# Optimization experiments

Hardware: AMD Instinct MI355X
Metric: run time of the kernel (lower is better)

## Reference

```python
import jax, jax.numpy as jnp
import numpy as np
from functools import partial

VOCAB, EMB, HID, B, T, K = 30000, 256, 512, 128, 256, 12
START, STOP = 10, 11


def lstm_scan(xs, mask, W_ih, W_hh, b_ih, b_hh, h0, c0):
    """xs: [T,B,E], mask: [T,B] bool. PyTorch gate order i,f,g,o. Masked steps carry state (packed-seq semantics)."""
    def step(carry, inp):
        h, c = carry
        x_t, m_t = inp
        gates = x_t @ W_ih.T + h @ W_hh.T + (b_ih + b_hh)  # [B,4H]
        i, f, g, o = jnp.split(gates, 4, axis=-1)
        c_new = jax.nn.sigmoid(f) * c + jax.nn.sigmoid(i) * jnp.tanh(g)
        h_new = jax.nn.sigmoid(o) * jnp.tanh(c_new)
        m = m_t[:, None]
        h = jnp.where(m, h_new, h)
        c = jnp.where(m, c_new, c)
        return (h, c), h
    _, hs = jax.lax.scan(step, (h0, c0), (xs, mask))
    return hs  # [T,B,H]


def crf_log_partition(emissions, mask, trans):
    """emissions: [T,B,K], mask: [T,B]. Vectorized log-sum-exp forward algorithm."""
    b, k = emissions.shape[1], emissions.shape[2]
    alpha0 = jnp.full((b, k), -10000.0, emissions.dtype).at[:, START].set(0.0)
    def step(alpha, inp):
        emit_t, m_t = inp
        # alpha_new[b,j] = logsumexp_i(alpha[b,i] + trans[j,i]) + emit[b,j]
        scores = alpha[:, None, :] + trans[None, :, :]  # [B,Knext,Kprev]
        alpha_new = jax.nn.logsumexp(scores, axis=-1) + emit_t
        return jnp.where(m_t[:, None], alpha_new, alpha), None
    alpha, _ = jax.lax.scan(step, alpha0, (emissions, mask))
    return jax.nn.logsumexp(alpha + trans[STOP][None, :], axis=-1)  # [B]


def crf_gold_score(emissions_bt, tags, lengths, trans):
    """emissions_bt: [B,T,K]. Gold path score with <start> prepended and <stop> transition."""
    b, t = tags.shape
    tags_ext = jnp.concatenate([jnp.full((b, 1), START, tags.dtype), tags], axis=1)  # [B,T+1]
    prev, nxt = tags_ext[:, :-1], tags_ext[:, 1:]  # [B,T]
    trans_s = trans[nxt, prev]  # [B,T]
    emit_s = jnp.take_along_axis(emissions_bt, nxt[:, :, None], axis=2)[:, :, 0]  # [B,T]
    valid = jnp.arange(t)[None, :] < lengths[:, None]  # [B,T]
    score = jnp.sum(jnp.where(valid, trans_s + emit_s, 0.0), axis=1)
    last_tag = jnp.take_along_axis(tags, (lengths - 1)[:, None], axis=1)[:, 0]
    return score + trans[STOP, last_tag]


def setup_inputs() -> dict:
    key = jax.random.key(0)
    ks = jax.random.split(key, 16)
    s = 0.1
    x = jax.random.randint(ks[0], (B, T), 0, VOCAB)
    lengths = jax.random.randint(ks[1], (B,), 1, T + 1)
    tags = jax.random.randint(ks[2], (B, T), 0, K - 2)  # real labels only
    embedding = jax.random.normal(ks[3], (VOCAB, EMB), jnp.float32) * s
    W_ih_f = jax.random.normal(ks[4], (4 * HID, EMB), jnp.float32) * s
    W_hh_f = jax.random.normal(ks[5], (4 * HID, HID), jnp.float32) * s
    b_ih_f = jax.random.normal(ks[6], (4 * HID,), jnp.float32) * s
    b_hh_f = jax.random.normal(ks[7], (4 * HID,), jnp.float32) * s
    W_ih_b = jax.random.normal(ks[8], (4 * HID, EMB), jnp.float32) * s
    W_hh_b = jax.random.normal(ks[9], (4 * HID, HID), jnp.float32) * s
    b_ih_b = jax.random.normal(ks[10], (4 * HID,), jnp.float32) * s
    b_hh_b = jax.random.normal(ks[11], (4 * HID,), jnp.float32) * s
    fc_W = jax.random.normal(ks[12], (K, 2 * HID), jnp.float32) * s
    fc_b = jnp.zeros((K,), jnp.float32)
    trans = jax.random.normal(ks[13], (K, K), jnp.float32) * s
    trans = trans.at[START, :].set(-10000.0).at[:, STOP].set(-10000.0)
    h0 = jax.random.normal(ks[14], (2, B, HID), jnp.float32) * s
    c0 = jax.random.normal(ks[15], (2, B, HID), jnp.float32) * s
    return dict(x=x, lengths=lengths, tags=tags, embedding=embedding,
                W_ih_f=W_ih_f, W_hh_f=W_hh_f, b_ih_f=b_ih_f, b_hh_f=b_hh_f,
                W_ih_b=W_ih_b, W_hh_b=W_hh_b, b_ih_b=b_ih_b, b_hh_b=b_hh_b,
                fc_W=fc_W, fc_b=fc_b, trans=trans, h0=h0, c0=c0)


def reference(x, lengths, tags, embedding, W_ih_f, W_hh_f, b_ih_f, b_hh_f,
              W_ih_b, W_hh_b, b_ih_b, b_hh_b, fc_W, fc_b, trans, h0, c0):
    # neg_log_likelihood: BiLSTM emission feats -> CRF logZ - gold score. Dropout = eval (identity).
    emb = embedding[x]                 # [B,T,E]
    xs = emb.transpose(1, 0, 2)        # [T,B,E] time-major
    t = xs.shape[0]
    mask = jnp.arange(t)[:, None] < lengths[None, :]  # [T,B]
    hs_f = lstm_scan(xs, mask, W_ih_f, W_hh_f, b_ih_f, b_hh_f, h0[0], c0[0])
    hs_b = lstm_scan(xs[::-1], mask[::-1], W_ih_b, W_hh_b, b_ih_b, b_hh_b, h0[1], c0[1])[::-1]
    out = jnp.concatenate([hs_f, hs_b], axis=-1)      # [T,B,2H]
    emissions = out @ fc_W.T + fc_b                    # [T,B,K]
    log_z = crf_log_partition(emissions, mask, trans)  # [B]
    gold = crf_gold_score(emissions.transpose(1, 0, 2), tags, lengths, trans)  # [B]
    return log_z - gold  # per-sentence NLL, [B]
```

## Files before the change

### kernel.cpp

```cpp
#include <hip/hip_runtime.h>
#include <hip/hip_bf16.h>

#define TT 256
#define BB 128
#define EMBD 256
#define HID 512
#define KTAG 12
#define START_TAG 10
#define STOP_TAG 11
#define SMEM_BYTES 148608

typedef __attribute__((ext_vector_type(8))) short short8;
typedef __attribute__((ext_vector_type(4))) float f32x4;

__device__ __forceinline__ unsigned short f2bf(float f) {
    union { float f; unsigned int u; } v; v.f = f;
    unsigned int r = v.u + 0x7fffu + ((v.u >> 16) & 1u);
    return (unsigned short)(r >> 16);
}
__device__ __forceinline__ float fsig(float x) {
    return __fdividef(1.0f, 1.0f + __expf(-x));
}
__device__ __forceinline__ float ftanh(float x) {
    return 2.0f * __fdividef(1.0f, 1.0f + __expf(-2.0f * x)) - 1.0f;
}
__device__ __forceinline__ void gll16(const void* g, void* l) {
    __builtin_amdgcn_global_load_lds((const __attribute__((address_space(1))) void*)g,
                                     (__attribute__((address_space(3))) void*)l, 16, 0, 0);
}
__device__ __forceinline__ void pack8(const float* src, unsigned short* dst) {
    float4 v0 = *(const float4*)src;
    float4 v1 = *(const float4*)(src + 4);
    unsigned short tmp[8];
    tmp[0] = f2bf(v0.x); tmp[1] = f2bf(v0.y); tmp[2] = f2bf(v0.z); tmp[3] = f2bf(v0.w);
    tmp[4] = f2bf(v1.x); tmp[5] = f2bf(v1.y); tmp[6] = f2bf(v1.z); tmp[7] = f2bf(v1.w);
    *(uint4*)dst = *(const uint4*)tmp;
}

#define SCHED_FENCE() __builtin_amdgcn_sched_barrier(0)
#define WAIT_VM4() do { asm volatile("s_waitcnt vmcnt(4)" ::: "memory"); SCHED_FENCE(); } while (0)
#define WAIT_VM0() do { asm volatile("s_waitcnt vmcnt(0)" ::: "memory"); SCHED_FENCE(); } while (0)
#define BARRIER_RAW() do { __builtin_amdgcn_s_barrier(); SCHED_FENCE(); } while (0)

__global__ void prologue(const int* __restrict__ x, const float* __restrict__ emb,
                         const float* __restrict__ Wihf, const float* __restrict__ Whhf,
                         const float* __restrict__ Wihb, const float* __restrict__ Whhb,
                         const float* __restrict__ h0,
                         const float* __restrict__ bihf, const float* __restrict__ bhhf,
                         const float* __restrict__ bihb, const float* __restrict__ bhhb,
                         const float* __restrict__ fcW,
                         unsigned short* __restrict__ xs, unsigned short* __restrict__ Wr,
                         unsigned short* __restrict__ h0buf, float* __restrict__ bias2,
                         unsigned short* __restrict__ fcWr, unsigned int* __restrict__ ctrl)
{
    int blk = blockIdx.x;
    int tid = threadIdx.x;
    if (blk < 4096) {
        int i = blk * 256 + tid;
        int chk = i & 31;
        int row = i >> 5;
        int b = row & (BB - 1);
        int t = row >> 7;
        pack8(emb + (size_t)x[b * TT + t] * EMBD + chk * 8, xs + (size_t)row * EMBD + chk * 8);
    } else if (blk < 5632) {
        int i = (blk - 4096) * 256 + tid;
        int c8 = i % 96;
        int r2 = i / 96;
        int nr = r2 & 2047;
        int dir = r2 >> 11;
        int utile = nr >> 6;
        int r6 = nr & 63;
        int wm = r6 >> 4;
        int rr = r6 & 15;
        int ul = rr >> 2, g = rr & 3;
        int orow = g * HID + utile * 16 + wm * 4 + ul;
        int k0 = c8 * 8;
        const float* Wih = dir ? Wihb : Wihf;
        const float* Whh = dir ? Whhb : Whhf;
        const float* src = (k0 < EMBD) ? (Wih + (size_t)orow * EMBD + k0)
                                       : (Whh + (size_t)orow * HID + (k0 - EMBD));
        pack8(src, Wr + ((size_t)dir * 2048 + nr) * 768 + k0);
    } else {
        int i = (blk - 5632) * 256 + tid;
        if (i < 2 * BB * HID) h0buf[i] = f2bf(h0[i]);
        if (i < 2 * 2048) {
            int dir = i >> 11, j = i & 2047;
            bias2[i] = dir ? (bihb[j] + bhhb[j]) : (bihf[j] + bhhf[j]);
        }
        if (i < 16 * 1024) {
            int tag = i >> 10, k = i & 1023;
            fcWr[i] = f2bf(tag < KTAG ? fcW[tag * 1024 + k] : 0.0f);
        }
        if (i < 2048) ctrl[i] = 0u;
    }
}

__launch_bounds__(256, 1)
__global__ void lstm_persistent(
    const unsigned short* __restrict__ xs, const unsigned short* __restrict__ Wr,
    const float* __restrict__ bias2, const int* __restrict__ lengths,
    const unsigned short* __restrict__ h0buf, const float* __restrict__ c0,
    unsigned short* __restrict__ hsf, unsigned short* __restrict__ hsb,
    unsigned int* __restrict__ ctrl)
{
    extern __shared__ char smem[];
    unsigned short* Wlds = (unsigned short*)smem;
    unsigned short* Abuf = (unsigned short*)(smem + 98304);
    unsigned short* hrep = (unsigned short*)(smem + 147456);

    const int blk = blockIdx.x;
    const int grp = blk & 7;
    const int dir = grp >> 2;
    const int btile = grp & 3;
    const int utile = blk >> 3;
    const int bg0 = btile * 32;

    const int tid = threadIdx.x;
    const int w = tid >> 6;
    const int l = tid & 63;
    const int l15 = l & 15, l16 = l >> 4;

    unsigned int* wflags = ctrl + 64 + grp * 128;
    unsigned int* myflag = wflags + utile * 4 + w;

    unsigned short* hs = dir ? hsb : hsf;
    unsigned int* hs_u32 = (unsigned int*)hs;

    {
        const unsigned short* src0 =
            Wr + ((size_t)(dir * 2048 + utile * 64) + (w * 16 + l15)) * 768 + l16 * 8;
        #pragma unroll
        for (int ks = 0; ks < 24; ks++)
            gll16(src0 + ks * 32, Wlds + (w * 24 + ks) * 512);
    }
    {
        int mm = w & 1, ksb = (w >> 1) * 4;
        const int t0 = dir ? (TT - 1) : 0;
        const unsigned short* asrc =
            xs + ((size_t)t0 * BB + (bg0 + mm * 16 + l15)) * EMBD + l16 * 8;
        #pragma unroll
        for (int q = 0; q < 4; q++)
            gll16(asrc + (ksb + q) * 32, Abuf + (mm * 24 + ksb + q) * 512);
    }

    const int u = utile * 16 + w * 4 + l16;
    const int bA = bg0 + l15, bB = bg0 + 16 + l15;
    const int lenA = lengths[bA], lenB = lengths[bB];
    float cA = c0[((size_t)dir * BB + bA) * HID + u];
    float cB = c0[((size_t)dir * BB + bB) * HID + u];
    float bias_r[4];
    #pragma unroll
    for (int g = 0; g < 4; g++) bias_r[g] = bias2[dir * 2048 + g * 512 + u];

    for (int s = 0; s < TT; s++) {
        const int t = dir ? (TT - 1 - s) : s;

        __syncthreads();

        f32x4 aA0 = {bias_r[0], bias_r[1], bias_r[2], bias_r[3]};
        f32x4 aB0 = {bias_r[0], bias_r[1], bias_r[2], bias_r[3]};
        f32x4 aA1 = {0.f,0.f,0.f,0.f}, aB1 = {0.f,0.f,0.f,0.f};
        auto mstep = [&](int ks, f32x4& xA, f32x4& xB) {
            short8 a  = *(const short8*)(Wlds + ((w * 24 + ks) << 9) + (l << 3));
            short8 b0 = *(const short8*)(Abuf + (ks << 9) + (l << 3));
            short8 b1 = *(const short8*)(Abuf + ((24 + ks) << 9) + (l << 3));
            xA = __builtin_amdgcn_mfma_f32_16x16x32_bf16(a, b0, xA, 0, 0, 0);
            xB = __builtin_amdgcn_mfma_f32_16x16x32_bf16(a, b1, xB, 0, 0, 0);
        };
        #pragma unroll
        for (int ks = 0; ks < 8; ks += 2) { mstep(ks, aA0, aB0); mstep(ks + 1, aA1, aB1); }

        if (s > 0) {
            if (tid < 64) {
                unsigned tgt = (unsigned)s;
                const unsigned long long* fp =
                    (const unsigned long long*)(wflags + 2 * (tid & 63));
                unsigned long long v0 = __hip_atomic_load(fp, __ATOMIC_RELAXED,
                                                          __HIP_MEMORY_SCOPE_AGENT);
                unsigned long long v1 = __hip_atomic_load(fp, __ATOMIC_RELAXED,
                                                          __HIP_MEMORY_SCOPE_AGENT);
                while (true) {
                    bool ok = ((unsigned)v0 >= tgt) && ((unsigned)(v0 >> 32) >= tgt);
                    if (__all(ok)) break;
                    v0 = v1;
                    v1 = __hip_atomic_load(fp, __ATOMIC_RELAXED, __HIP_MEMORY_SCOPE_AGENT);
                }
            }
            __syncthreads();
        }
        const unsigned short* hsrc = (s == 0)
            ? (h0buf + (size_t)dir * BB * HID)
            : (hs + (size_t)(dir ? (t + 1) : (t - 1)) * BB * HID);

        {
            int mm = w & 1, ksb = 8 + (w >> 1) * 8;
            const unsigned short* asrcH = hsrc + (size_t)(bg0 + mm * 16 + l15) * HID + l16 * 8;
            #pragma unroll
            for (int q = 0; q < 8; q++)
                gll16(asrcH + ((ksb + q) * 32 - 256), Abuf + (mm * 24 + ksb + q) * 512);
        }
        SCHED_FENCE();
        WAIT_VM4();
        BARRIER_RAW();
        #pragma unroll
        for (int q = 0; q < 4; q++) { mstep(8 + q, aA0, aB0); mstep(16 + q, aA1, aB1); }
        WAIT_VM0();
        BARRIER_RAW();
        #pragma unroll
        for (int q = 0; q < 4; q++) { mstep(12 + q, aA0, aB0); mstep(20 + q, aA1, aB1); }
        f32x4 accA = aA0 + aA1;
        f32x4 accB = aB0 + aB1;

        {
            const int ksn = 8 + (u >> 5), kin = u & 31;
            const int baseA = ksn * 512 + ((kin >> 3) * 16 + l15) * 8 + (kin & 7);
            const int baseB = (24 + ksn) * 512 + ((kin >> 3) * 16 + l15) * 8 + (kin & 7);
            float cnA = fsig(accA[1]) * cA + fsig(accA[0]) * ftanh(accA[2]);
            float hnA = fsig(accA[3]) * ftanh(cnA);
            float cnB = fsig(accB[1]) * cB + fsig(accB[0]) * ftanh(accB[2]);
            float hnB = fsig(accB[3]) * ftanh(cnB);
            bool mA = t < lenA, mB = t < lenB;
            unsigned short hvA = mA ? f2bf(hnA) : Abuf[baseA];
            unsigned short hvB = mB ? f2bf(hnB) : Abuf[baseB];
            cA = mA ? cnA : cA;
            cB = mB ? cnB : cB;
            hrep[l15 * 18 + w * 4 + l16]        = hvA;
            hrep[(16 + l15) * 18 + w * 4 + l16] = hvB;
        }
        __syncthreads();

        {
            int bl = tid >> 3, up = tid & 7;
            unsigned v0 = hrep[bl * 18 + up * 2];
            unsigned v1 = hrep[bl * 18 + up * 2 + 1];
            unsigned pk = v0 | (v1 << 16);
            size_t widx = (((size_t)t * BB + (bg0 + bl)) * HID + utile * 16 + up * 2) >> 1;
            __hip_atomic_store(hs_u32 + widx, pk, __ATOMIC_RELAXED, __HIP_MEMORY_SCOPE_AGENT);
        }
        SCHED_FENCE();
        if (s < TT - 1) {
            const int tn = dir ? (TT - 2 - s) : (s + 1);
            int mm = w & 1, ksb = (w >> 1) * 4;
            const unsigned short* asrc =
                xs + ((size_t)tn * BB + (bg0 + mm * 16 + l15)) * EMBD + l16 * 8;
            #pragma unroll
            for (int q = 0; q < 4; q++)
                gll16(asrc + (ksb + q) * 32, Abuf + (mm * 24 + ksb + q) * 512);
            SCHED_FENCE();
            WAIT_VM4();
            if (l == 0)
                __hip_atomic_store(myflag, (unsigned)(s + 1), __ATOMIC_RELAXED,
                                   __HIP_MEMORY_SCOPE_AGENT);
        }
    }
}

__global__ void emissions_mfma(const unsigned short* __restrict__ hsf,
                               const unsigned short* __restrict__ hsb,
                               const unsigned short* __restrict__ fcWr,
                               const float* __restrict__ fcb, float* __restrict__ emis)
{
    int wid = (blockIdx.x * blockDim.x + threadIdx.x) >> 6;
    int l = threadIdx.x & 63;
    int l15 = l & 15, l16 = l >> 4;
    int rowbase = wid * 16;
    f32x4 acc0 = {0.f,0.f,0.f,0.f}, acc1 = {0.f,0.f,0.f,0.f};
    auto estep = [&](const unsigned short* hsp, int ks, f32x4& acc) {
        short8 av = *(const short8*)(hsp + (size_t)(rowbase + l15) * HID + (ks & 15) * 32 + l16 * 8);
        short8 bv = *(const short8*)(fcWr + l15 * 1024 + ks * 32 + l16 * 8);
        acc = __builtin_amdgcn_mfma_f32_16x16x32_bf16(av, bv, acc, 0, 0, 0);
    };
    #pragma unroll
    for (int ks = 0; ks < 16; ks += 2) { estep(hsf, ks, acc0); estep(hsf, ks + 1, acc1); }
    #pragma unroll
    for (int ks = 16; ks < 32; ks += 2) { estep(hsb, ks, acc0); estep(hsb, ks + 1, acc1); }
    f32x4 acc = acc0 + acc1;
    float bval = fcb[l15 < KTAG ? l15 : 0];
    if (l15 < KTAG) {
        #pragma unroll
        for (int r = 0; r < 4; r++)
            emis[(size_t)(rowbase + 4 * l16 + r) * KTAG + l15] = acc[r] + bval;
    }
}

__global__ void crf_gold(const float* __restrict__ emis, const int* __restrict__ lengths,
                         const int* __restrict__ tags, const float* __restrict__ trans,
                         float* __restrict__ out)
{
    __shared__ float s_logz, s_gold;
    int b = blockIdx.x;
    int tid = threadIdx.x;
    int len = lengths[b];
    if (tid < 64) {
        int lane = tid;
        float trow[KTAG];
        #pragma unroll
        for (int j = 0; j < KTAG; j++)
            trow[j] = (lane < KTAG) ? trans[lane * KTAG + j] : -1e30f;
        float alpha = (lane == START_TAG) ? 0.0f : -10000.0f;
        float e_cur = (lane < KTAG) ? emis[(size_t)b * KTAG + lane] : 0.0f;
        for (int t = 0; t < len; t++) {
            int tn = (t + 1 < TT) ? t + 1 : t;
            float e_next = (lane < KTAG) ? emis[(size_t)(tn * BB + b) * KTAG + lane] : 0.0f;
            float sc[KTAG];
            #pragma unroll
            for (int j = 0; j < KTAG; j++) sc[j] = __shfl(alpha, j, 64) + trow[j];
            float m = sc[0];
            #pragma unroll
            for (int j = 1; j < KTAG; j++) m = fmaxf(m, sc[j]);
            float ssum = 0.0f;
            #pragma unroll
            for (int j = 0; j < KTAG; j++) ssum += __expf(sc[j] - m);
            float anew = m + __logf(ssum) + e_cur;
            alpha = (lane < KTAG) ? anew : alpha;
            e_cur = e_next;
        }
        float v = (lane < KTAG) ? (alpha + trans[STOP_TAG * KTAG + lane]) : -1e30f;
        float m = v;
        #pragma unroll
        for (int off = 1; off < 16; off <<= 1) m = fmaxf(m, __shfl_xor(m, off, 64));
        float e = __expf(v - m);
        #pragma unroll
        for (int off = 1; off < 16; off <<= 1) e += __shfl_xor(e, off, 64);
        if (lane == 0) s_logz = m + __logf(e);
    } else {
        int l2 = tid - 64;
        float part = 0.0f;
        #pragma unroll
        for (int q = 0; q < 4; q++) {
            int t = l2 + q * 64;
            if (t < len) {
                int nxt = tags[b * TT + t];
                int prev = t ? tags[b * TT + t - 1] : START_TAG;
                part += trans[nxt * KTAG + prev] + emis[(size_t)(t * BB + b) * KTAG + nxt];
            }
        }
        #pragma unroll
        for (int off = 1; off < 64; off <<= 1) part += __shfl_xor(part, off, 64);
        if (l2 == 0) s_gold = part + trans[STOP_TAG * KTAG + tags[b * TT + len - 1]];
    }
    __syncthreads();
    if (tid == 0) out[b] = s_logz - s_gold;
}

extern "C" void kernel_launch(void* const* d_in, const int* in_sizes, int n_in,
                              void* d_out, int out_size, void* d_ws, size_t ws_size,
                              hipStream_t stream)
{
    (void)in_sizes; (void)n_in; (void)out_size; (void)ws_size;
    const int*   x     = (const int*)d_in[0];
    const int*   lens  = (const int*)d_in[1];
    const int*   tags  = (const int*)d_in[2];
    const float* emb   = (const float*)d_in[3];
    const float* Wihf  = (const float*)d_in[4];
    const float* Whhf  = (const float*)d_in[5];
    const float* bihf  = (const float*)d_in[6];
    const float* bhhf  = (const float*)d_in[7];
    const float* Wihb  = (const float*)d_in[8];
    const float* Whhb  = (const float*)d_in[9];
    const float* bihb  = (const float*)d_in[10];
    const float* bhhb  = (const float*)d_in[11];
    const float* fcW   = (const float*)d_in[12];
    const float* fcb   = (const float*)d_in[13];
    const float* trans = (const float*)d_in[14];
    const float* h0    = (const float*)d_in[15];
    const float* c0    = (const float*)d_in[16];
    float* out = (float*)d_out;

    char* ws = (char*)d_ws;
    size_t off = 0;
    auto alloc = [&](size_t bytes) {
        void* p = ws + off;
        off += (bytes + 255) & ~(size_t)255;
        return p;
    };
    unsigned short* xs    = (unsigned short*)alloc((size_t)TT * BB * EMBD * 2);
    unsigned short* Wr    = (unsigned short*)alloc((size_t)2 * 2048 * 768 * 2);
    float*          bias2 = (float*)alloc((size_t)2 * 2048 * 4);
    unsigned short* h0buf = (unsigned short*)alloc((size_t)2 * BB * HID * 2);
    unsigned short* hsf   = (unsigned short*)alloc((size_t)TT * BB * HID * 2);
    unsigned short* hsb   = (unsigned short*)alloc((size_t)TT * BB * HID * 2);
    float*          emis  = (float*)alloc((size_t)TT * BB * KTAG * 4);
    unsigned short* fcWr  = (unsigned short*)alloc((size_t)16 * 1024 * 2);
    unsigned int*   ctrl  = (unsigned int*)alloc((size_t)2048 * 4);

    prologue<<<6144, 256, 0, stream>>>(x, emb, Wihf, Whhf, Wihb, Whhb, h0,
                                       bihf, bhhf, bihb, bhhb, fcW,
                                       xs, Wr, h0buf, bias2, fcWr, ctrl);

    hipFuncSetAttribute(reinterpret_cast<const void*>(lstm_persistent),
                        hipFuncAttributeMaxDynamicSharedMemorySize, SMEM_BYTES);
    {
        const unsigned short* p_xs = xs; const unsigned short* p_Wr = Wr;
        const float* p_bias2 = bias2; const int* p_lens = lens;
        const unsigned short* p_h0 = h0buf; const float* p_c0 = c0;
        unsigned short* p_hsf = hsf; unsigned short* p_hsb = hsb;
        unsigned int* p_ctrl = ctrl;
        void* args[9] = { &p_xs, &p_Wr, &p_bias2, &p_lens, &p_h0, &p_c0,
                          &p_hsf, &p_hsb, &p_ctrl };
        hipError_t e = hipLaunchCooperativeKernel(
            reinterpret_cast<const void*>(lstm_persistent),
            dim3(256), dim3(256), args, (unsigned)SMEM_BYTES, stream);
        if (e != hipSuccess) {
            lstm_persistent<<<256, 256, SMEM_BYTES, stream>>>(
                xs, Wr, bias2, lens, h0buf, c0, hsf, hsb, ctrl);
        }
    }

    emissions_mfma<<<512, 256, 0, stream>>>(hsf, hsb, fcWr, fcb, emis);
    crf_gold<<<BB, 128, 0, stream>>>(emis, lens, tags, trans, out);
}
```

Measured before the change: 1.071 ms.

## Skip padded timesteps per batch tile and use hierarchical flag barrier

Each batch tile now computes the maximum sequence length of its 32 sentences and runs the recurrence only for that many steps. For the backward direction it starts at that maximum instead of the last padded position, so fully masked steps are skipped. The all-to-all flag polling is replaced by a two-level barrier. Block utile 0 of each group polls all the per-wave flags, which are now padded to 64-byte slots, and then publishes a ready counter that the other blocks spin on with a single thread. This cuts redundant polling traffic and false sharing, at the cost of an extra hop of latency through the detector block. Hidden states past each tile's maximum length are left unwritten, which relies on the CRF and gold-score masking to ignore them.

```diff
diff --git a/kernel.cpp b/kernel.cpp
--- a/kernel.cpp
+++ b/kernel.cpp
@@ -91,7 +91,7 @@
             int tag = i >> 10, k = i & 1023;
             fcWr[i] = f2bf(tag < KTAG ? fcW[tag * 1024 + k] : 0.0f);
         }
-        if (i < 2048) ctrl[i] = 0u;
+        if (i < 24576) ctrl[i] = 0u;
     }
 }
 
@@ -107,6 +107,7 @@
     unsigned short* Wlds = (unsigned short*)smem;
     unsigned short* Abuf = (unsigned short*)(smem + 98304);
     unsigned short* hrep = (unsigned short*)(smem + 147456);
+    __shared__ int s_ml;
 
     const int blk = blockIdx.x;
     const int grp = blk & 7;
@@ -120,11 +121,24 @@
     const int l = tid & 63;
     const int l15 = l & 15, l16 = l >> 4;
 
-    unsigned int* wflags = ctrl + 64 + grp * 128;
-    unsigned int* myflag = wflags + utile * 4 + w;
+    unsigned int* flags  = ctrl + grp * 2048;
+    unsigned int* myflag = flags + (utile * 4 + w) * 16;
+    unsigned int* ready  = ctrl + 16384 + grp * 64;
+    const bool isDet = (utile == 0);
 
     unsigned short* hs = dir ? hsb : hsf;
     unsigned int* hs_u32 = (unsigned int*)hs;
+
+    {
+        int v = (tid < 32) ? lengths[bg0 + tid] : 0;
+        if (tid < 64) {
+            #pragma unroll
+            for (int off = 32; off >= 1; off >>= 1) v = max(v, __shfl_xor(v, off, 64));
+            if (tid == 0) s_ml = v;
+        }
+    }
+    __syncthreads();
+    const int TTs = s_ml;
 
     {
         const unsigned short* src0 =
@@ -135,7 +149,7 @@
     }
     {
         int mm = w & 1, ksb = (w >> 1) * 4;
-        const int t0 = dir ? (TT - 1) : 0;
+        const int t0 = dir ? (TTs - 1) : 0;
         const unsigned short* asrc =
             xs + ((size_t)t0 * BB + (bg0 + mm * 16 + l15)) * EMBD + l16 * 8;
         #pragma unroll
@@ -152,8 +166,8 @@
     #pragma unroll
     for (int g = 0; g < 4; g++) bias_r[g] = bias2[dir * 2048 + g * 512 + u];
 
-    for (int s = 0; s < TT; s++) {
-        const int t = dir ? (TT - 1 - s) : s;
+    for (int k = 0; k < TTs; k++) {
+        const int t = dir ? (TTs - 1 - k) : k;
 
         __syncthreads();
 
@@ -170,25 +184,33 @@
         #pragma unroll
         for (int ks = 0; ks < 8; ks += 2) { mstep(ks, aA0, aB0); mstep(ks + 1, aA1, aB1); }
 
-        if (s > 0) {
-            if (tid < 64) {
-                unsigned tgt = (unsigned)s;
-                const unsigned long long* fp =
-                    (const unsigned long long*)(wflags + 2 * (tid & 63));
-                unsigned long long v0 = __hip_atomic_load(fp, __ATOMIC_RELAXED,
-                                                          __HIP_MEMORY_SCOPE_AGENT);
-                unsigned long long v1 = __hip_atomic_load(fp, __ATOMIC_RELAXED,
-                                                          __HIP_MEMORY_SCOPE_AGENT);
-                while (true) {
-                    bool ok = ((unsigned)v0 >= tgt) && ((unsigned)(v0 >> 32) >= tgt);
-                    if (__all(ok)) break;
-                    v0 = v1;
-                    v1 = __hip_atomic_load(fp, __ATOMIC_RELAXED, __HIP_MEMORY_SCOPE_AGENT);
+        if (k > 0) {
+            unsigned tgt = (unsigned)k;
+            if (isDet) {
+                if (tid < 64) {
+                    const unsigned int* f0 = flags + tid * 16;
+                    const unsigned int* f1 = flags + (tid + 64) * 16;
+                    while (true) {
+                        unsigned a = __hip_atomic_load(f0, __ATOMIC_RELAXED,
+                                                       __HIP_MEMORY_SCOPE_AGENT);
+                        unsigned b = __hip_atomic_load(f1, __ATOMIC_RELAXED,
+                                                       __HIP_MEMORY_SCOPE_AGENT);
+                        if (__all(a >= tgt && b >= tgt)) break;
+                    }
+                    if (l < 4)
+                        __hip_atomic_store(ready + l * 16, tgt, __ATOMIC_RELAXED,
+                                           __HIP_MEMORY_SCOPE_AGENT);
+                }
+            } else {
+                if (tid == 0) {
+                    const unsigned int* rp = ready + (utile & 3) * 16;
+                    while (__hip_atomic_load(rp, __ATOMIC_RELAXED,
+                                             __HIP_MEMORY_SCOPE_AGENT) < tgt) { }
                 }
             }
             __syncthreads();
         }
-        const unsigned short* hsrc = (s == 0)
+        const unsigned short* hsrc = (k == 0)
             ? (h0buf + (size_t)dir * BB * HID)
             : (hs + (size_t)(dir ? (t + 1) : (t - 1)) * BB * HID);
 
@@ -238,8 +260,8 @@
             __hip_atomic_store(hs_u32 + widx, pk, __ATOMIC_RELAXED, __HIP_MEMORY_SCOPE_AGENT);
         }
         SCHED_FENCE();
-        if (s < TT - 1) {
-            const int tn = dir ? (TT - 2 - s) : (s + 1);
+        if (k < TTs - 1) {
+            const int tn = dir ? (TTs - 2 - k) : (k + 1);
             int mm = w & 1, ksb = (w >> 1) * 4;
             const unsigned short* asrc =
                 xs + ((size_t)tn * BB + (bg0 + mm * 16 + l15)) * EMBD + l16 * 8;
@@ -249,7 +271,7 @@
             SCHED_FENCE();
             WAIT_VM4();
             if (l == 0)
-                __hip_atomic_store(myflag, (unsigned)(s + 1), __ATOMIC_RELAXED,
+                __hip_atomic_store(myflag, (unsigned)(k + 1), __ATOMIC_RELAXED,
                                    __HIP_MEMORY_SCOPE_AGENT);
         }
     }
@@ -382,7 +404,7 @@
     unsigned short* hsb   = (unsigned short*)alloc((size_t)TT * BB * HID * 2);
     float*          emis  = (float*)alloc((size_t)TT * BB * KTAG * 4);
     unsigned short* fcWr  = (unsigned short*)alloc((size_t)16 * 1024 * 2);
-    unsigned int*   ctrl  = (unsigned int*)alloc((size_t)2048 * 4);
+    unsigned int*   ctrl  = (unsigned int*)alloc((size_t)32768 * 4);
 
     prologue<<<6144, 256, 0, stream>>>(x, emb, Wihf, Whhf, Wihb, Whhb, h0,
                                        bihf, bhhf, bihb, bhhb, fcW,
```

Result: slower. 2.783 ms (+159.8%).

## Stop LSTM recurrence at tile max length; stage fc weights in LDS

Applied to the files above, without the earlier changes.

Each batch tile now computes the maximum sequence length of its 32 sentences and runs the persistent LSTM recurrence only up to that length. The backward direction starts at that maximum instead of at T-1, which matches the reference because fully masked leading steps would only carry the initial state. This targets the serial per-timestep cost for padded positions. Hidden states beyond the maximum are never written, so correctness relies on downstream consumers masking those positions. Separately, the emissions kernel now copies the fc weights into shared memory once per block and has each wave handle two row tiles, with half as many blocks.

```diff
diff --git a/kernel.cpp b/kernel.cpp
--- a/kernel.cpp
+++ b/kernel.cpp
@@ -107,6 +107,7 @@
     unsigned short* Wlds = (unsigned short*)smem;
     unsigned short* Abuf = (unsigned short*)(smem + 98304);
     unsigned short* hrep = (unsigned short*)(smem + 147456);
+    __shared__ int s_ml;
 
     const int blk = blockIdx.x;
     const int grp = blk & 7;
@@ -127,6 +128,17 @@
     unsigned int* hs_u32 = (unsigned int*)hs;
 
     {
+        int v = (tid < 32) ? lengths[bg0 + tid] : 0;
+        if (tid < 64) {
+            #pragma unroll
+            for (int off = 32; off >= 1; off >>= 1) v = max(v, __shfl_xor(v, off, 64));
+            if (tid == 0) s_ml = v;
+        }
+    }
+    __syncthreads();
+    const int TTs = s_ml;
+
+    {
         const unsigned short* src0 =
             Wr + ((size_t)(dir * 2048 + utile * 64) + (w * 16 + l15)) * 768 + l16 * 8;
         #pragma unroll
@@ -135,7 +147,7 @@
     }
     {
         int mm = w & 1, ksb = (w >> 1) * 4;
-        const int t0 = dir ? (TT - 1) : 0;
+        const int t0 = dir ? (TTs - 1) : 0;
         const unsigned short* asrc =
             xs + ((size_t)t0 * BB + (bg0 + mm * 16 + l15)) * EMBD + l16 * 8;
         #pragma unroll
@@ -152,8 +164,8 @@
     #pragma unroll
     for (int g = 0; g < 4; g++) bias_r[g] = bias2[dir * 2048 + g * 512 + u];
 
-    for (int s = 0; s < TT; s++) {
-        const int t = dir ? (TT - 1 - s) : s;
+    for (int k = 0; k < TTs; k++) {
+        const int t = dir ? (TTs - 1 - k) : k;
 
         __syncthreads();
 
@@ -170,9 +182,9 @@
         #pragma unroll
         for (int ks = 0; ks < 8; ks += 2) { mstep(ks, aA0, aB0); mstep(ks + 1, aA1, aB1); }
 
-        if (s > 0) {
+        if (k > 0) {
             if (tid < 64) {
-                unsigned tgt = (unsigned)s;
+                unsigned tgt = (unsigned)k;
                 const unsigned long long* fp =
                     (const unsigned long long*)(wflags + 2 * (tid & 63));
                 unsigned long long v0 = __hip_atomic_load(fp, __ATOMIC_RELAXED,
@@ -188,7 +200,7 @@
             }
             __syncthreads();
         }
-        const unsigned short* hsrc = (s == 0)
+        const unsigned short* hsrc = (k == 0)
             ? (h0buf + (size_t)dir * BB * HID)
             : (hs + (size_t)(dir ? (t + 1) : (t - 1)) * BB * HID);
 
@@ -238,8 +250,8 @@
             __hip_atomic_store(hs_u32 + widx, pk, __ATOMIC_RELAXED, __HIP_MEMORY_SCOPE_AGENT);
         }
         SCHED_FENCE();
-        if (s < TT - 1) {
-            const int tn = dir ? (TT - 2 - s) : (s + 1);
+        if (k < TTs - 1) {
+            const int tn = dir ? (TTs - 2 - k) : (k + 1);
             int mm = w & 1, ksb = (w >> 1) * 4;
             const unsigned short* asrc =
                 xs + ((size_t)tn * BB + (bg0 + mm * 16 + l15)) * EMBD + l16 * 8;
@@ -249,7 +261,7 @@
             SCHED_FENCE();
             WAIT_VM4();
             if (l == 0)
-                __hip_atomic_store(myflag, (unsigned)(s + 1), __ATOMIC_RELAXED,
+                __hip_atomic_store(myflag, (unsigned)(k + 1), __ATOMIC_RELAXED,
                                    __HIP_MEMORY_SCOPE_AGENT);
         }
     }
@@ -260,26 +272,36 @@
                                const unsigned short* __restrict__ fcWr,
                                const float* __restrict__ fcb, float* __restrict__ emis)
 {
-    int wid = (blockIdx.x * blockDim.x + threadIdx.x) >> 6;
-    int l = threadIdx.x & 63;
+    __shared__ unsigned short Wl[16 * 1024];
+    int tid = threadIdx.x;
+    #pragma unroll
+    for (int p = 0; p < 8; p++) {
+        int i = (p * 256 + tid) * 8;
+        *(uint4*)(Wl + i) = *(const uint4*)(fcWr + i);
+    }
+    __syncthreads();
+    int w = tid >> 6, l = tid & 63;
     int l15 = l & 15, l16 = l >> 4;
-    int rowbase = wid * 16;
-    f32x4 acc0 = {0.f,0.f,0.f,0.f}, acc1 = {0.f,0.f,0.f,0.f};
-    auto estep = [&](const unsigned short* hsp, int ks, f32x4& acc) {
-        short8 av = *(const short8*)(hsp + (size_t)(rowbase + l15) * HID + (ks & 15) * 32 + l16 * 8);
-        short8 bv = *(const short8*)(fcWr + l15 * 1024 + ks * 32 + l16 * 8);
-        acc = __builtin_amdgcn_mfma_f32_16x16x32_bf16(av, bv, acc, 0, 0, 0);
-    };
+    float bval = fcb[l15 < KTAG ? l15 : 0];
     #pragma unroll
-    for (int ks = 0; ks < 16; ks += 2) { estep(hsf, ks, acc0); estep(hsf, ks + 1, acc1); }
-    #pragma unroll
-    for (int ks = 16; ks < 32; ks += 2) { estep(hsb, ks, acc0); estep(hsb, ks + 1, acc1); }
-    f32x4 acc = acc0 + acc1;
-    float bval = fcb[l15 < KTAG ? l15 : 0];
-    if (l15 < KTAG) {
-        #pragma unroll
-        for (int r = 0; r < 4; r++)
-            emis[(size_t)(rowbase + 4 * l16 + r) * KTAG + l15] = acc[r] + bval;
+    for (int tile = 0; tile < 2; tile++) {
+        int rowbase = ((blockIdx.x * 4 + w) * 2 + tile) * 16;
+        f32x4 acc0 = {0.f,0.f,0.f,0.f}, acc1 = {0.f,0.f,0.f,0.f};
+        auto estep = [&](const unsigned short* hsp, int ks, f32x4& acc) {
+            short8 av = *(const short8*)(hsp + (size_t)(rowbase + l15) * HID + (ks & 15) * 32 + l16 * 8);
+            short8 bv = *(const short8*)(Wl + l15 * 1024 + ks * 32 + l16 * 8);
+            acc = __builtin_amdgcn_mfma_f32_16x16x32_bf16(av, bv, acc, 0, 0, 0);
+        };
+        #pragma unroll
+        for (int ks = 0; ks < 16; ks += 2) { estep(hsf, ks, acc0); estep(hsf, ks + 1, acc1); }
+        #pragma unroll
+        for (int ks = 16; ks < 32; ks += 2) { estep(hsb, ks, acc0); estep(hsb, ks + 1, acc1); }
+        f32x4 acc = acc0 + acc1;
+        if (l15 < KTAG) {
+            #pragma unroll
+            for (int r = 0; r < 4; r++)
+                emis[(size_t)(rowbase + 4 * l16 + r) * KTAG + l15] = acc[r] + bval;
+        }
     }
 }
 
@@ -407,6 +429,6 @@
         }
     }
 
-    emissions_mfma<<<512, 256, 0, stream>>>(hsf, hsb, fcWr, fcb, emis);
+    emissions_mfma<<<256, 256, 0, stream>>>(hsf, hsb, fcWr, fcb, emis);
     crf_gold<<<BB, 128, 0, stream>>>(emis, lens, tags, trans, out);
 }
```

Result: slower. 2.719 ms (+153.8%).
